# Kernel optimization log

Hardware: AMD Instinct MI355X
Metric: run time of the kernel (lower is better)

Reference implementation:

```python
import jax, jax.numpy as jnp
import numpy as np

HID = 4096
BLOCK = 64


def _masks(n=HID, bs=BLOCK):
    blk = jnp.arange(n) // bs
    mask_diag = (blk[:, None] == blk[None, :]).astype(jnp.float32)  # block-diagonal ones
    triu = (jnp.arange(n)[:, None] <= jnp.arange(n)[None, :]).astype(jnp.float32)
    mask_triu = triu * (1.0 - mask_diag)  # strictly above-block upper triangle
    return mask_diag, mask_triu


def _mc_linear(x, W, b, mask_diag, mask_triu):
    # A uses detached input (stop_gradient); B carries gradient through x.
    A = jax.lax.stop_gradient(x) @ (W * mask_triu)
    B = x @ (W * mask_diag)
    return A + B + b


def setup_inputs() -> dict:
    key = jax.random.key(0)
    ks = jax.random.split(key, 10)
    X = jax.random.normal(ks[0], (8192, 1024), dtype=jnp.float32)
    s_in = 1.0 / np.sqrt(1024)
    s_h = 1.0 / np.sqrt(HID)
    W0 = jax.random.normal(ks[1], (1024, HID), dtype=jnp.float32) * s_in
    b0 = jax.random.normal(ks[2], (HID,), dtype=jnp.float32) * s_in
    W1 = jax.random.normal(ks[3], (HID, HID), dtype=jnp.float32) * s_h
    b1 = jax.random.normal(ks[4], (HID,), dtype=jnp.float32) * s_h
    W2 = jax.random.normal(ks[5], (HID, HID), dtype=jnp.float32) * s_h
    b2 = jax.random.normal(ks[6], (HID,), dtype=jnp.float32) * s_h
    W3 = jax.random.normal(ks[7], (HID, HID), dtype=jnp.float32) * s_h
    b3 = jax.random.normal(ks[8], (HID,), dtype=jnp.float32) * s_h
    return {"X": X, "W0": W0, "b0": b0, "W1": W1, "b1": b1,
            "W2": W2, "b2": b2, "W3": W3, "b3": b3}


def reference(X, W0, b0, W1, b1, W2, b2, W3, b3):
    mask_diag, mask_triu = _masks()
    h = X @ W0 + b0  # [B, HID]
    for W, b in ((W1, b1), (W2, b2), (W3, b3)):
        h = jax.nn.relu(h)  # dropout=0.0 -> identity
        h = _mc_linear(h, W, b, mask_diag, mask_triu)
    y_pred = h[..., BLOCK - 1::BLOCK]  # [B, num_blocks]
    return y_pred[..., -1]  # level = -1 (default LEVEL)
```

## Files before the change

kernel.cpp:

```cpp
#include <hip/hip_runtime.h>

typedef unsigned short u16;
typedef __attribute__((ext_vector_type(8))) short short8;
typedef __attribute__((ext_vector_type(4))) float f32x4;
typedef __attribute__((ext_vector_type(4))) unsigned short us4;

__device__ __forceinline__ u16 f2bf(float f) {
    unsigned u = __float_as_uint(f);
    u += 0x7fffu + ((u >> 16) & 1u);
    return (u16)(u >> 16);
}
__device__ __forceinline__ float bf2f(u16 h) {
    return __uint_as_float(((unsigned)h) << 16);
}

__global__ __launch_bounds__(256) void k_cvt(const float* __restrict__ in,
                                             u16* __restrict__ out, long n) {
    long i = ((long)blockIdx.x * 256 + threadIdx.x) * 4;
    if (i >= n) return;
    float4 v = *(const float4*)(in + i);
    us4 o;
    o.x = f2bf(v.x); o.y = f2bf(v.y); o.z = f2bf(v.z); o.w = f2bf(v.w);
    *(us4*)(out + i) = o;
}

__global__ __launch_bounds__(256) void k_transpose(const float* __restrict__ W,
                                                   u16* __restrict__ Wt,
                                                   int K, int N, int mask) {
    __shared__ float tile[32][33];
    const int n0 = blockIdx.x * 32, k0 = blockIdx.y * 32;
    const int tx = threadIdx.x, ty = threadIdx.y;
    if (mask && ((k0 >> 6) > (n0 >> 6))) {
        if (k0 >= ((n0 >> 8) + 1) * 256) return;
#pragma unroll
        for (int j = 0; j < 32; j += 8)
            Wt[(size_t)(n0 + ty + j) * K + (k0 + tx)] = 0;
        return;
    }
#pragma unroll
    for (int j = 0; j < 32; j += 8)
        tile[ty + j][tx] = W[(size_t)(k0 + ty + j) * N + (n0 + tx)];
    __syncthreads();
#pragma unroll
    for (int j = 0; j < 32; j += 8)
        Wt[(size_t)(n0 + ty + j) * K + (k0 + tx)] = f2bf(tile[tx][ty + j]);
}

__global__ __launch_bounds__(256) void k_extract(const float* __restrict__ W3,
                                                 float* __restrict__ col, int N) {
    int k = blockIdx.x * 256 + threadIdx.x;
    col[k] = W3[(size_t)k * N + (N - 1)];
}

#define BM 256
#define BN 256
#define BK 32
#define BUFE 16384
#define GLDS(src, dst)                                                          \
    __builtin_amdgcn_global_load_lds(                                           \
        (const __attribute__((address_space(1))) void*)(src),                   \
        (__attribute__((address_space(3))) void*)(dst), 16, 0, 0)

__global__ __launch_bounds__(512, 2) void k_gemm(const u16* __restrict__ A,
                                                 const u16* __restrict__ Bt,
                                                 const float* __restrict__ bias,
                                                 u16* __restrict__ C,
                                                 int M, int N, int K, int varK) {
    __shared__ __align__(16) u16 lds[4 * BUFE];

    const int d = blockIdx.y * gridDim.x + blockIdx.x;
    int bx, by;
    if (varK) {
        bx = (int)gridDim.x - 1 - (d / (int)gridDim.y);
        by = d % (int)gridDim.y;
    } else {
        const int nwg = (int)(gridDim.x * gridDim.y);
        const int cpx = nwg >> 3;
        const int swz = (d & 7) * cpx + (d >> 3);
        bx = swz % (int)gridDim.x;
        by = swz / (int)gridDim.x;
    }

    const int tid = (int)threadIdx.x;
    const int lane = tid & 63, wv = tid >> 6;
    const int wm = wv >> 2, wn = wv & 3;
    const int keff = varK ? min(K, (bx + 1) * BN) : K;
    const int nt = keff >> 5;

    const u16* Ab = A + (size_t)by * BM * K;
    const u16* Bb = Bt + (size_t)bx * BN * K;

    const int c0 = tid, c1 = tid + 512;
    const int ar0 = c0 >> 2, as0 = ((c0 & 3) ^ ((c0 >> 3) & 3)) * 8;
    const int ar1 = c1 >> 2, as1 = ((c1 & 3) ^ ((c1 >> 3) & 3)) * 8;
    const u16* pA0 = Ab + (size_t)ar0 * K + as0;
    const u16* pA1 = Ab + (size_t)ar1 * K + as1;
    const u16* pB0 = Bb + (size_t)ar0 * K + as0;
    const u16* pB1 = Bb + (size_t)ar1 * K + as1;
    u16* dA0 = lds + c0 * 8;
    u16* dA1 = lds + c1 * 8;
    u16* dB0 = lds + 8192 + c0 * 8;
    u16* dB1 = lds + 8192 + c1 * 8;

    const int l15 = lane & 15;
    const int sl8 = (((lane >> 4) ^ ((l15 >> 1) & 3))) * 8;
    const int aoff = (wm * 128 + l15) * BK + sl8;
    const int boff = 8192 + (wn * 64 + l15) * BK + sl8;

#define STAGE(t)                                                      \
    {                                                                 \
        const size_t o = (size_t)(t)*BK;                              \
        const int b = ((t)&3) * BUFE;                                 \
        GLDS(pA0 + o, dA0 + b); GLDS(pA1 + o, dA1 + b);               \
        GLDS(pB0 + o, dB0 + b); GLDS(pB1 + o, dB1 + b);               \
    }
#define DSREAD(t, af, bf)                                             \
    {                                                                 \
        const int b = ((t)&3) * BUFE;                                 \
        _Pragma("unroll")                                             \
        for (int mf = 0; mf < 8; ++mf)                                \
            af[mf] = *(const short8*)(lds + b + aoff + mf * 512);     \
        _Pragma("unroll")                                             \
        for (int nf = 0; nf < 4; ++nf)                                \
            bf[nf] = *(const short8*)(lds + b + boff + nf * 512);     \
    }
#define MFMA_SET(af, bf)                                              \
    {                                                                 \
        __builtin_amdgcn_s_setprio(1);                                \
        _Pragma("unroll")                                             \
        for (int mf = 0; mf < 8; ++mf)                                \
            _Pragma("unroll")                                         \
            for (int nf = 0; nf < 4; ++nf)                            \
                acc[mf][nf] = __builtin_amdgcn_mfma_f32_16x16x32_bf16(\
                    af[mf], bf[nf], acc[mf][nf], 0, 0, 0);            \
        __builtin_amdgcn_s_setprio(0);                                \
    }
#define WAITBAR4  asm volatile("s_waitcnt vmcnt(4)\n\ts_barrier" ::: "memory")
#define WAITBAR0  asm volatile("s_waitcnt vmcnt(0)\n\ts_barrier" ::: "memory")

    f32x4 acc[8][4];
#pragma unroll
    for (int i = 0; i < 8; ++i)
#pragma unroll
        for (int j = 0; j < 4; ++j)
            acc[i][j] = (f32x4){0.f, 0.f, 0.f, 0.f};

    short8 afA[8], bfA[4], afB[8], bfB[4];

    STAGE(0); STAGE(1); STAGE(2);
    WAITBAR4;
    DSREAD(0, afA, bfA);

    for (int t = 0; t < nt; t += 2) {
        if (t + 3 < nt) STAGE(t + 3);
        DSREAD(t + 1, afB, bfB);
        MFMA_SET(afA, bfA);
        if (t + 3 < nt) WAITBAR4; else WAITBAR0;
        const int u = t + 1;
        if (u + 3 < nt) STAGE(u + 3);
        if (u + 1 < nt) DSREAD(u + 1, afA, bfA);
        MFMA_SET(afB, bfB);
        if (u + 1 < nt) { if (u + 3 < nt) WAITBAR4; else WAITBAR0; }
    }

    const int rbase = by * BM + wm * 128 + (lane >> 4) * 4;
    const int cbase = bx * BN + wn * 64 + l15;
#pragma unroll
    for (int nf = 0; nf < 4; ++nf) {
        const int gc = cbase + nf * 16;
        const float bv = bias[gc];
#pragma unroll
        for (int mf = 0; mf < 8; ++mf) {
#pragma unroll
            for (int r = 0; r < 4; ++r) {
                int gr = rbase + mf * 16 + r;
                float h = acc[mf][nf][r] + bv;
                h = fmaxf(h, 0.0f);
                C[(size_t)gr * N + gc] = f2bf(h);
            }
        }
    }
#undef STAGE
#undef DSREAD
#undef MFMA_SET
#undef WAITBAR4
#undef WAITBAR0
}

__global__ __launch_bounds__(256) void k_matvec(const u16* __restrict__ act,
                                                const float* __restrict__ col,
                                                const float* __restrict__ b3,
                                                float* __restrict__ out, int K) {
    const int m = blockIdx.x, t = (int)threadIdx.x;
    const u16* row = act + (size_t)m * K;
    float acc = 0.f;
#pragma unroll
    for (int j = 0; j < 2; ++j) {
        int base = t * 16 + j * 8;
        short8 v = *(const short8*)(row + base);
#pragma unroll
        for (int u = 0; u < 8; ++u)
            acc += bf2f((u16)v[u]) * col[base + u];
    }
#pragma unroll
    for (int off = 32; off > 0; off >>= 1)
        acc += __shfl_down(acc, off);
    __shared__ float red[4];
    if ((t & 63) == 0) red[t >> 6] = acc;
    __syncthreads();
    if (t == 0) out[m] = red[0] + red[1] + red[2] + red[3] + b3[K - 1];
}

extern "C" void kernel_launch(void* const* d_in, const int* in_sizes, int n_in,
                              void* d_out, int out_size, void* d_ws, size_t ws_size,
                              hipStream_t stream) {
    const float* X  = (const float*)d_in[0];
    const float* W0 = (const float*)d_in[1];
    const float* b0 = (const float*)d_in[2];
    const float* W1 = (const float*)d_in[3];
    const float* b1 = (const float*)d_in[4];
    const float* W2 = (const float*)d_in[5];
    const float* b2 = (const float*)d_in[6];
    const float* W3 = (const float*)d_in[7];
    const float* b3 = (const float*)d_in[8];
    float* out = (float*)d_out;

    const int M = 8192, K0 = 1024, H = 4096;

    char* ws = (char*)d_ws;
    u16* Wt    = (u16*)(ws);
    u16* actA  = (u16*)(ws + 33554432);
    u16* actB  = (u16*)(ws + 33554432 + 67108864);
    u16* Xb    = actB;
    float* col = (float*)(ws + 33554432 + 2 * 67108864);

    k_cvt<<<dim3((M * K0) / 1024), 256, 0, stream>>>(X, Xb, (long)M * K0);
    k_transpose<<<dim3(H / 32, K0 / 32), dim3(32, 8), 0, stream>>>(W0, Wt, K0, H, 0);
    k_gemm<<<dim3(H / BN, M / BM), 512, 0, stream>>>(Xb, Wt, b0, actA, M, H, K0, 0);
    k_transpose<<<dim3(H / 32, H / 32), dim3(32, 8), 0, stream>>>(W1, Wt, H, H, 1);
    k_gemm<<<dim3(H / BN, M / BM), 512, 0, stream>>>(actA, Wt, b1, actB, M, H, H, 1);
    k_transpose<<<dim3(H / 32, H / 32), dim3(32, 8), 0, stream>>>(W2, Wt, H, H, 1);
    k_gemm<<<dim3(H / BN, M / BM), 512, 0, stream>>>(actB, Wt, b2, actA, M, H, H, 1);
    k_extract<<<dim3(H / 256), 256, 0, stream>>>(W3, col, H);
    k_matvec<<<dim3(M), 256, 0, stream>>>(actA, col, b3, out, H);
}
```

Baseline: 413.0 us.

## Restructure GEMM main loop to BK=64 double buffer with interleaved sub-stage loads

Raises the K-tile from 32 to 64 and replaces the 4-deep BK=32 ring with a 2-buffer BK=64 scheme. Each tile is split into four MFMA quarter-steps, and the global-to-LDS loads for the next tile (A chunks, and B for the tile after) are interleaved between them with finer barriers. It also uses a new 8-way XOR LDS swizzle. The aim is fewer barrier round-trips per K element and better overlap of loads with MFMA. The cost is more barriers per tile and a more fragile scheduling of buffer reuse hazards.

```diff
diff --git a/kernel.cpp b/kernel.cpp
--- a/kernel.cpp
+++ b/kernel.cpp
@@ -54,8 +54,7 @@
 
 #define BM 256
 #define BN 256
-#define BK 32
-#define BUFE 16384
+#define BK 64
 #define GLDS(src, dst)                                                          \
     __builtin_amdgcn_global_load_lds(                                           \
         (const __attribute__((address_space(1))) void*)(src),                   \
@@ -66,7 +65,7 @@
                                                  const float* __restrict__ bias,
                                                  u16* __restrict__ C,
                                                  int M, int N, int K, int varK) {
-    __shared__ __align__(16) u16 lds[4 * BUFE];
+    __shared__ __align__(16) u16 lds[2 * 32768];
 
     const int d = blockIdx.y * gridDim.x + blockIdx.x;
     int bx, by;
@@ -85,58 +84,58 @@
     const int lane = tid & 63, wv = tid >> 6;
     const int wm = wv >> 2, wn = wv & 3;
     const int keff = varK ? min(K, (bx + 1) * BN) : K;
-    const int nt = keff >> 5;
+    const int nt = keff >> 6;
 
     const u16* Ab = A + (size_t)by * BM * K;
     const u16* Bb = Bt + (size_t)bx * BN * K;
 
-    const int c0 = tid, c1 = tid + 512;
-    const int ar0 = c0 >> 2, as0 = ((c0 & 3) ^ ((c0 >> 3) & 3)) * 8;
-    const int ar1 = c1 >> 2, as1 = ((c1 & 3) ^ ((c1 >> 3) & 3)) * 8;
-    const u16* pA0 = Ab + (size_t)ar0 * K + as0;
-    const u16* pA1 = Ab + (size_t)ar1 * K + as1;
-    const u16* pB0 = Bb + (size_t)ar0 * K + as0;
-    const u16* pB1 = Bb + (size_t)ar1 * K + as1;
-    u16* dA0 = lds + c0 * 8;
-    u16* dA1 = lds + c1 * 8;
-    u16* dB0 = lds + 8192 + c0 * 8;
-    u16* dB1 = lds + 8192 + c1 * 8;
+    const int tr = tid >> 3, ts = tid & 7;
+    const int ss = ts ^ (tr & 7);
+    const u16* aSrc = Ab + (size_t)tr * K + ss * 8;
+    const u16* bSrc = Bb + (size_t)tr * K + ss * 8;
+
+#define STA(tt, ci, dbuf) GLDS(aSrc + (size_t)(tt) * BK + (size_t)(ci) * 64 * K, \
+                               lds + (dbuf) + (ci) * 4096 + tid * 8)
+#define STB(tt, ci, dbuf) GLDS(bSrc + (size_t)(tt) * BK + (size_t)(ci) * 64 * K, \
+                               lds + (dbuf) + 16384 + (ci) * 4096 + tid * 8)
 
     const int l15 = lane & 15;
-    const int sl8 = (((lane >> 4) ^ ((l15 >> 1) & 3))) * 8;
-    const int aoff = (wm * 128 + l15) * BK + sl8;
-    const int boff = 8192 + (wn * 64 + l15) * BK + sl8;
-
-#define STAGE(t)                                                      \
-    {                                                                 \
-        const size_t o = (size_t)(t)*BK;                              \
-        const int b = ((t)&3) * BUFE;                                 \
-        GLDS(pA0 + o, dA0 + b); GLDS(pA1 + o, dA1 + b);               \
-        GLDS(pB0 + o, dB0 + b); GLDS(pB1 + o, dB1 + b);               \
-    }
-#define DSREAD(t, af, bf)                                             \
-    {                                                                 \
-        const int b = ((t)&3) * BUFE;                                 \
-        _Pragma("unroll")                                             \
-        for (int mf = 0; mf < 8; ++mf)                                \
-            af[mf] = *(const short8*)(lds + b + aoff + mf * 512);     \
-        _Pragma("unroll")                                             \
-        for (int nf = 0; nf < 4; ++nf)                                \
-            bf[nf] = *(const short8*)(lds + b + boff + nf * 512);     \
-    }
-#define MFMA_SET(af, bf)                                              \
-    {                                                                 \
-        __builtin_amdgcn_s_setprio(1);                                \
-        _Pragma("unroll")                                             \
-        for (int mf = 0; mf < 8; ++mf)                                \
-            _Pragma("unroll")                                         \
-            for (int nf = 0; nf < 4; ++nf)                            \
-                acc[mf][nf] = __builtin_amdgcn_mfma_f32_16x16x32_bf16(\
-                    af[mf], bf[nf], acc[mf][nf], 0, 0, 0);            \
-        __builtin_amdgcn_s_setprio(0);                                \
-    }
-#define WAITBAR4  asm volatile("s_waitcnt vmcnt(4)\n\ts_barrier" ::: "memory")
-#define WAITBAR0  asm volatile("s_waitcnt vmcnt(0)\n\ts_barrier" ::: "memory")
+    const int sw = (lane >> 4) ^ (l15 & 7);
+    const int arow = wm * 128 + l15;
+    const int brow = wn * 64 + l15;
+
+#define RDA(dst, mfh, ks, dbuf)                                                        \
+    {                                                                                  \
+        _Pragma("unroll")                                                              \
+        for (int i = 0; i < 4; ++i)                                                    \
+            dst[i] = *(const short8*)(lds + (dbuf) + (arow + (mfh) * 64 + i * 16) * 64 \
+                                      + ((sw ^ ((ks) << 2))) * 8);                     \
+    }
+#define RDB(dst, ks, dbuf)                                                             \
+    {                                                                                  \
+        _Pragma("unroll")                                                              \
+        for (int nf = 0; nf < 4; ++nf)                                                 \
+            dst[nf] = *(const short8*)(lds + (dbuf) + 16384 + (brow + nf * 16) * 64    \
+                                       + ((sw ^ ((ks) << 2))) * 8);                    \
+    }
+#define MFMA16(afS, bfS, mb)                                                           \
+    {                                                                                  \
+        __builtin_amdgcn_s_setprio(1);                                                 \
+        _Pragma("unroll")                                                              \
+        for (int i = 0; i < 4; ++i)                                                    \
+            _Pragma("unroll")                                                          \
+            for (int nf = 0; nf < 4; ++nf)                                             \
+                acc[(mb) + i][nf] = __builtin_amdgcn_mfma_f32_16x16x32_bf16(           \
+                    afS[i], bfS[nf], acc[(mb) + i][nf], 0, 0, 0);                      \
+        __builtin_amdgcn_s_setprio(0);                                                 \
+    }
+#define MIDSYNC                                                   \
+    __builtin_amdgcn_s_barrier();                                 \
+    asm volatile("s_waitcnt lgkmcnt(0)" ::: "memory");            \
+    __builtin_amdgcn_sched_barrier(0);
+#define ENDSYNC                                                   \
+    asm volatile("s_waitcnt vmcnt(2)" ::: "memory");              \
+    __builtin_amdgcn_s_barrier();
 
     f32x4 acc[8][4];
 #pragma unroll
@@ -145,22 +144,43 @@
         for (int j = 0; j < 4; ++j)
             acc[i][j] = (f32x4){0.f, 0.f, 0.f, 0.f};
 
-    short8 afA[8], bfA[4], afB[8], bfB[4];
-
-    STAGE(0); STAGE(1); STAGE(2);
-    WAITBAR4;
-    DSREAD(0, afA, bfA);
-
-    for (int t = 0; t < nt; t += 2) {
-        if (t + 3 < nt) STAGE(t + 3);
-        DSREAD(t + 1, afB, bfB);
-        MFMA_SET(afA, bfA);
-        if (t + 3 < nt) WAITBAR4; else WAITBAR0;
-        const int u = t + 1;
-        if (u + 3 < nt) STAGE(u + 3);
-        if (u + 1 < nt) DSREAD(u + 1, afA, bfA);
-        MFMA_SET(afB, bfB);
-        if (u + 1 < nt) { if (u + 3 < nt) WAITBAR4; else WAITBAR0; }
+    short8 afX[4], afY[4], bfA[4], bfB[4];
+
+    STA(0, 0, 0); STA(0, 2, 0); STA(0, 1, 0); STA(0, 3, 0);
+    STB(0, 0, 0); STB(0, 1, 0); STB(0, 2, 0); STB(0, 3, 0);
+    STB(1, 0, 32768); STB(1, 1, 32768); STB(1, 2, 32768); STB(1, 3, 32768);
+    asm volatile("s_waitcnt vmcnt(4)" ::: "memory");
+    __builtin_amdgcn_s_barrier();
+    RDA(afX, 0, 0, 0);
+    RDB(bfA, 0, 0);
+
+    for (int T = 0; T < nt; ++T) {
+        const int bT = (T & 1) << 15;
+        const int bNx = bT ^ 32768;
+        RDA(afY, 1, 0, bT);
+        if (T + 1 < nt) { STA(T + 1, 0, bNx); STA(T + 1, 2, bNx); }
+        MIDSYNC;
+        MFMA16(afX, bfA, 0);
+        ENDSYNC;
+        RDA(afX, 0, 1, bT);
+        RDB(bfB, 1, bT);
+        if (T + 1 < nt) { STA(T + 1, 1, bNx); STA(T + 1, 3, bNx); }
+        MIDSYNC;
+        MFMA16(afY, bfA, 4);
+        ENDSYNC;
+        RDA(afY, 1, 1, bT);
+        if (T + 2 < nt) { STB(T + 2, 0, bT); STB(T + 2, 1, bT); }
+        MIDSYNC;
+        MFMA16(afX, bfB, 0);
+        ENDSYNC;
+        if (T + 1 < nt) {
+            RDA(afX, 0, 0, bNx);
+            RDB(bfA, 0, bNx);
+        }
+        if (T + 2 < nt) { STB(T + 2, 2, bT); STB(T + 2, 3, bT); }
+        MIDSYNC;
+        MFMA16(afY, bfB, 4);
+        ENDSYNC;
     }
 
     const int rbase = by * BM + wm * 128 + (lane >> 4) * 4;
@@ -180,11 +200,13 @@
             }
         }
     }
-#undef STAGE
-#undef DSREAD
-#undef MFMA_SET
-#undef WAITBAR4
-#undef WAITBAR0
+#undef STA
+#undef STB
+#undef RDA
+#undef RDB
+#undef MFMA16
+#undef MIDSYNC
+#undef ENDSYNC
 }
 
 __global__ __launch_bounds__(256) void k_matvec(const u16* __restrict__ act,
```

After: 387.4 us. -6.2%, faster.

## Split GEMM main loop into four half-tile phases with interleaved loads

Applied to the files above, without the earlier changes.

Restructures the bf16 MFMA GEMM main loop so that each K-tile is processed in two half-M phases. Each phase has its own LDS reads, global-to-LDS stages and barriers, so A and B global loads are spread across phases and interleaved with smaller 16-MFMA groups. This keeps fewer fragment registers live (4 A fragments at a time instead of 8) and is meant to improve overlap of memory traffic with compute, at the cost of more barriers per tile. The LDS swizzle and addressing are also recomputed in a different form.

```diff
diff --git a/kernel.cpp b/kernel.cpp
--- a/kernel.cpp
+++ b/kernel.cpp
@@ -90,53 +90,52 @@
     const u16* Ab = A + (size_t)by * BM * K;
     const u16* Bb = Bt + (size_t)bx * BN * K;
 
-    const int c0 = tid, c1 = tid + 512;
-    const int ar0 = c0 >> 2, as0 = ((c0 & 3) ^ ((c0 >> 3) & 3)) * 8;
-    const int ar1 = c1 >> 2, as1 = ((c1 & 3) ^ ((c1 >> 3) & 3)) * 8;
-    const u16* pA0 = Ab + (size_t)ar0 * K + as0;
-    const u16* pA1 = Ab + (size_t)ar1 * K + as1;
-    const u16* pB0 = Bb + (size_t)ar0 * K + as0;
-    const u16* pB1 = Bb + (size_t)ar1 * K + as1;
-    u16* dA0 = lds + c0 * 8;
-    u16* dA1 = lds + c1 * 8;
-    u16* dB0 = lds + 8192 + c0 * 8;
-    u16* dB1 = lds + 8192 + c1 * 8;
+    const int tr = tid >> 2, ts = tid & 3;
+    const int ss = ts ^ ((tr >> 1) & 3);
+    const u16* aSrc = Ab + (size_t)tr * K + ss * 8;
+    const u16* bSrc = Bb + (size_t)tr * K + ss * 8;
+
+#define STA(tt, ci, dbuf) GLDS(aSrc + (size_t)(tt) * BK + (size_t)(ci) * 128 * K, \
+                               lds + (dbuf) + (ci) * 4096 + tid * 8)
+#define STB(tt, ci, dbuf) GLDS(bSrc + (size_t)(tt) * BK + (size_t)(ci) * 128 * K, \
+                               lds + (dbuf) + 8192 + (ci) * 4096 + tid * 8)
 
     const int l15 = lane & 15;
-    const int sl8 = (((lane >> 4) ^ ((l15 >> 1) & 3))) * 8;
-    const int aoff = (wm * 128 + l15) * BK + sl8;
-    const int boff = 8192 + (wn * 64 + l15) * BK + sl8;
-
-#define STAGE(t)                                                      \
-    {                                                                 \
-        const size_t o = (size_t)(t)*BK;                              \
-        const int b = ((t)&3) * BUFE;                                 \
-        GLDS(pA0 + o, dA0 + b); GLDS(pA1 + o, dA1 + b);               \
-        GLDS(pB0 + o, dB0 + b); GLDS(pB1 + o, dB1 + b);               \
-    }
-#define DSREAD(t, af, bf)                                             \
-    {                                                                 \
-        const int b = ((t)&3) * BUFE;                                 \
-        _Pragma("unroll")                                             \
-        for (int mf = 0; mf < 8; ++mf)                                \
-            af[mf] = *(const short8*)(lds + b + aoff + mf * 512);     \
-        _Pragma("unroll")                                             \
-        for (int nf = 0; nf < 4; ++nf)                                \
-            bf[nf] = *(const short8*)(lds + b + boff + nf * 512);     \
-    }
-#define MFMA_SET(af, bf)                                              \
-    {                                                                 \
-        __builtin_amdgcn_s_setprio(1);                                \
-        _Pragma("unroll")                                             \
-        for (int mf = 0; mf < 8; ++mf)                                \
-            _Pragma("unroll")                                         \
-            for (int nf = 0; nf < 4; ++nf)                            \
-                acc[mf][nf] = __builtin_amdgcn_mfma_f32_16x16x32_bf16(\
-                    af[mf], bf[nf], acc[mf][nf], 0, 0, 0);            \
-        __builtin_amdgcn_s_setprio(0);                                \
-    }
-#define WAITBAR4  asm volatile("s_waitcnt vmcnt(4)\n\ts_barrier" ::: "memory")
-#define WAITBAR0  asm volatile("s_waitcnt vmcnt(0)\n\ts_barrier" ::: "memory")
+    const int sw = (lane >> 4) ^ ((l15 >> 1) & 3);
+    const int arow = wm * 128 + l15;
+    const int brow = wn * 64 + l15;
+
+#define RDA(dst, mfh, dbuf)                                                          \
+    {                                                                                \
+        _Pragma("unroll")                                                            \
+        for (int i = 0; i < 4; ++i)                                                  \
+            dst[i] = *(const short8*)(lds + (dbuf) + (arow + (mfh) * 64 + i * 16) * 32 \
+                                      + sw * 8);                                     \
+    }
+#define RDB(dst, dbuf)                                                               \
+    {                                                                                \
+        _Pragma("unroll")                                                            \
+        for (int nf = 0; nf < 4; ++nf)                                               \
+            dst[nf] = *(const short8*)(lds + (dbuf) + 8192 + (brow + nf * 16) * 32   \
+                                       + sw * 8);                                    \
+    }
+#define MFMA16(afS, bfS, mb)                                                         \
+    {                                                                                \
+        __builtin_amdgcn_s_setprio(1);                                              \
+        _Pragma("unroll")                                                            \
+        for (int i = 0; i < 4; ++i)                                                  \
+            _Pragma("unroll")                                                        \
+            for (int nf = 0; nf < 4; ++nf)                                           \
+                acc[(mb) + i][nf] = __builtin_amdgcn_mfma_f32_16x16x32_bf16(         \
+                    afS[i], bfS[nf], acc[(mb) + i][nf], 0, 0, 0);                    \
+        __builtin_amdgcn_s_setprio(0);                                              \
+    }
+#define PHASE_END                                                 \
+    __builtin_amdgcn_sched_barrier(0);                            \
+    asm volatile("s_barrier" ::: "memory");
+#define VMW6 asm volatile("s_waitcnt vmcnt(6)" ::: "memory")
+#define VMW4 asm volatile("s_waitcnt vmcnt(4)" ::: "memory")
+#define VMW0 asm volatile("s_waitcnt vmcnt(0)" ::: "memory")
 
     f32x4 acc[8][4];
 #pragma unroll
@@ -145,22 +144,47 @@
         for (int j = 0; j < 4; ++j)
             acc[i][j] = (f32x4){0.f, 0.f, 0.f, 0.f};
 
-    short8 afA[8], bfA[4], afB[8], bfB[4];
-
-    STAGE(0); STAGE(1); STAGE(2);
-    WAITBAR4;
-    DSREAD(0, afA, bfA);
-
-    for (int t = 0; t < nt; t += 2) {
-        if (t + 3 < nt) STAGE(t + 3);
-        DSREAD(t + 1, afB, bfB);
-        MFMA_SET(afA, bfA);
-        if (t + 3 < nt) WAITBAR4; else WAITBAR0;
-        const int u = t + 1;
-        if (u + 3 < nt) STAGE(u + 3);
-        if (u + 1 < nt) DSREAD(u + 1, afA, bfA);
-        MFMA_SET(afB, bfB);
-        if (u + 1 < nt) { if (u + 3 < nt) WAITBAR4; else WAITBAR0; }
+    short8 afX[4], afY[4], bfP[4], bfQ[4];
+
+    STA(0, 0, 0);     STA(0, 1, 0);     STB(0, 0, 0);     STB(0, 1, 0);
+    STA(1, 0, BUFE);  STA(1, 1, BUFE);  STB(1, 0, BUFE);  STB(1, 1, BUFE);
+    STA(2, 0, 2*BUFE);STA(2, 1, 2*BUFE);STB(2, 0, 2*BUFE);STB(2, 1, 2*BUFE);
+    asm volatile("s_waitcnt vmcnt(8)" ::: "memory");
+    asm volatile("s_barrier" ::: "memory");
+    RDA(afX, 0, 0);
+    RDB(bfP, 0);
+
+    for (int T = 0; T < nt; T += 2) {
+        const int U = T + 1;
+        const int bT = (T & 3) * BUFE;
+        const int bU = ((T + 1) & 3) * BUFE;
+        const int bV = ((T + 2) & 3) * BUFE;
+        const int bZ1 = ((T + 3) & 3) * BUFE;
+        const int bZ2 = ((T + 4) & 3) * BUFE;
+        RDA(afY, 1, bT);
+        if (T + 3 < nt) { STA(T + 3, 0, bZ1); STA(T + 3, 1, bZ1); }
+        MFMA16(afX, bfP, 0);
+        if (T + 3 < nt) { VMW6; } else { VMW0; }
+        PHASE_END;
+        RDA(afX, 0, bU);
+        RDB(bfQ, bU);
+        if (T + 3 < nt) { STB(T + 3, 0, bZ1); STB(T + 3, 1, bZ1); }
+        MFMA16(afY, bfP, 4);
+        PHASE_END;
+        RDA(afY, 1, bU);
+        if (U + 3 < nt) { STA(U + 3, 0, bZ2); STA(U + 3, 1, bZ2); }
+        MFMA16(afX, bfQ, 0);
+        if (U + 1 < nt) {
+            if (U + 3 < nt) { VMW6; } else if (U + 2 < nt) { VMW4; } else { VMW0; }
+        }
+        PHASE_END;
+        if (U + 1 < nt) {
+            RDA(afX, 0, bV);
+            RDB(bfP, bV);
+        }
+        if (U + 3 < nt) { STB(U + 3, 0, bZ2); STB(U + 3, 1, bZ2); }
+        MFMA16(afY, bfQ, 4);
+        PHASE_END;
     }
 
     const int rbase = by * BM + wm * 128 + (lane >> 4) * 4;
@@ -180,11 +204,15 @@
             }
         }
     }
-#undef STAGE
-#undef DSREAD
-#undef MFMA_SET
-#undef WAITBAR4
-#undef WAITBAR0
+#undef STA
+#undef STB
+#undef RDA
+#undef RDB
+#undef MFMA16
+#undef PHASE_END
+#undef VMW6
+#undef VMW4
+#undef VMW0
 }
 
 __global__ __launch_bounds__(256) void k_matvec(const u16* __restrict__ act,
```

Result: faster. 393.2 us (-4.8%).

## Restructure GEMM main loop into BK=64 double buffer with quarter-phase interleaving

Applied to the files above, without the earlier changes.

Replaces the 4-stage BK=32 LDS ring with a 2-buffer BK=64 layout split into half-K slabs. Each K tile runs as four phases that interleave LDS reads, async global-to-LDS stages and quarter-tile MFMA blocks, separated by explicit barriers and sched_barriers. It keeps a smaller fragment register set live (4 A fragments instead of 16). The aim is finer overlap of loads with compute and lower register pressure, at the cost of many more workgroup barriers per iteration and tighter prefetch timing.

```diff
diff --git a/kernel.cpp b/kernel.cpp
--- a/kernel.cpp
+++ b/kernel.cpp
@@ -54,8 +54,8 @@
 
 #define BM 256
 #define BN 256
-#define BK 32
-#define BUFE 16384
+#define BK 64
+#define BUFE 32768
 #define GLDS(src, dst)                                                          \
     __builtin_amdgcn_global_load_lds(                                           \
         (const __attribute__((address_space(1))) void*)(src),                   \
@@ -66,7 +66,7 @@
                                                  const float* __restrict__ bias,
                                                  u16* __restrict__ C,
                                                  int M, int N, int K, int varK) {
-    __shared__ __align__(16) u16 lds[4 * BUFE];
+    __shared__ __align__(16) u16 lds[2 * BUFE];
 
     const int d = blockIdx.y * gridDim.x + blockIdx.x;
     int bx, by;
@@ -85,58 +85,66 @@
     const int lane = tid & 63, wv = tid >> 6;
     const int wm = wv >> 2, wn = wv & 3;
     const int keff = varK ? min(K, (bx + 1) * BN) : K;
-    const int nt = keff >> 5;
+    const int nt = keff >> 6;
 
     const u16* Ab = A + (size_t)by * BM * K;
     const u16* Bb = Bt + (size_t)bx * BN * K;
 
-    const int c0 = tid, c1 = tid + 512;
-    const int ar0 = c0 >> 2, as0 = ((c0 & 3) ^ ((c0 >> 3) & 3)) * 8;
-    const int ar1 = c1 >> 2, as1 = ((c1 & 3) ^ ((c1 >> 3) & 3)) * 8;
-    const u16* pA0 = Ab + (size_t)ar0 * K + as0;
-    const u16* pA1 = Ab + (size_t)ar1 * K + as1;
-    const u16* pB0 = Bb + (size_t)ar0 * K + as0;
-    const u16* pB1 = Bb + (size_t)ar1 * K + as1;
-    u16* dA0 = lds + c0 * 8;
-    u16* dA1 = lds + c1 * 8;
-    u16* dB0 = lds + 8192 + c0 * 8;
-    u16* dB1 = lds + 8192 + c1 * 8;
+    const int srow = tid >> 2, sslot = tid & 3;
+    const int ss = sslot ^ ((srow >> 1) & 3);
+    const u16* aSrc0 = Ab + (size_t)srow * K + ss * 8;
+    const u16* aSrc1 = Ab + (size_t)(srow + 128) * K + ss * 8;
+    const u16* bSrc0 = Bb + (size_t)srow * K + ss * 8;
+    const u16* bSrc1 = Bb + (size_t)(srow + 128) * K + ss * 8;
+
+#define STGA(tt, kh)                                                            \
+    {                                                                           \
+        const int db = (((tt) & 1) * BUFE) + (kh) * 8192;                       \
+        const size_t so = (size_t)(tt) * 64 + (kh) * 32;                        \
+        GLDS(aSrc0 + so, lds + db + tid * 8);                                   \
+        GLDS(aSrc1 + so, lds + db + 4096 + tid * 8);                            \
+    }
+#define STGB(tt, kh)                                                            \
+    {                                                                           \
+        const int db = (((tt) & 1) * BUFE) + 16384 + (kh) * 8192;               \
+        const size_t so = (size_t)(tt) * 64 + (kh) * 32;                        \
+        GLDS(bSrc0 + so, lds + db + tid * 8);                                   \
+        GLDS(bSrc1 + so, lds + db + 4096 + tid * 8);                            \
+    }
 
     const int l15 = lane & 15;
-    const int sl8 = (((lane >> 4) ^ ((l15 >> 1) & 3))) * 8;
-    const int aoff = (wm * 128 + l15) * BK + sl8;
-    const int boff = 8192 + (wn * 64 + l15) * BK + sl8;
-
-#define STAGE(t)                                                      \
-    {                                                                 \
-        const size_t o = (size_t)(t)*BK;                              \
-        const int b = ((t)&3) * BUFE;                                 \
-        GLDS(pA0 + o, dA0 + b); GLDS(pA1 + o, dA1 + b);               \
-        GLDS(pB0 + o, dB0 + b); GLDS(pB1 + o, dB1 + b);               \
-    }
-#define DSREAD(t, af, bf)                                             \
-    {                                                                 \
-        const int b = ((t)&3) * BUFE;                                 \
-        _Pragma("unroll")                                             \
-        for (int mf = 0; mf < 8; ++mf)                                \
-            af[mf] = *(const short8*)(lds + b + aoff + mf * 512);     \
-        _Pragma("unroll")                                             \
-        for (int nf = 0; nf < 4; ++nf)                                \
-            bf[nf] = *(const short8*)(lds + b + boff + nf * 512);     \
-    }
-#define MFMA_SET(af, bf)                                              \
-    {                                                                 \
-        __builtin_amdgcn_s_setprio(1);                                \
-        _Pragma("unroll")                                             \
-        for (int mf = 0; mf < 8; ++mf)                                \
-            _Pragma("unroll")                                         \
-            for (int nf = 0; nf < 4; ++nf)                            \
-                acc[mf][nf] = __builtin_amdgcn_mfma_f32_16x16x32_bf16(\
-                    af[mf], bf[nf], acc[mf][nf], 0, 0, 0);            \
-        __builtin_amdgcn_s_setprio(0);                                \
-    }
-#define WAITBAR4  asm volatile("s_waitcnt vmcnt(4)\n\ts_barrier" ::: "memory")
-#define WAITBAR0  asm volatile("s_waitcnt vmcnt(0)\n\ts_barrier" ::: "memory")
+    const int sw = (lane >> 4) ^ ((l15 >> 1) & 3);
+    const int arow = wm * 128 + l15;
+    const int brow = wn * 64 + l15;
+
+#define RDA(mh, ks, bT)                                                         \
+    {                                                                           \
+        _Pragma("unroll")                                                       \
+        for (int i = 0; i < 4; ++i)                                             \
+            af[i] = *(const short8*)(lds + (bT) + (ks) * 8192 +                  \
+                                     (arow + (mh) * 64 + i * 16) * 32 + sw * 8);\
+    }
+#define RDB(ks, bT)                                                             \
+    {                                                                           \
+        _Pragma("unroll")                                                       \
+        for (int nf = 0; nf < 4; ++nf)                                          \
+            bf[nf] = *(const short8*)(lds + (bT) + 16384 + (ks) * 8192 +        \
+                                      (brow + nf * 16) * 32 + sw * 8);          \
+    }
+#define MFMAQ(mh)                                                               \
+    {                                                                           \
+        __builtin_amdgcn_s_setprio(1);                                          \
+        _Pragma("unroll")                                                       \
+        for (int i = 0; i < 4; ++i)                                             \
+            _Pragma("unroll")                                                   \
+            for (int nf = 0; nf < 4; ++nf)                                      \
+                acc[(mh) * 4 + i][nf] = __builtin_amdgcn_mfma_f32_16x16x32_bf16(\
+                    af[i], bf[nf], acc[(mh) * 4 + i][nf], 0, 0, 0);             \
+        __builtin_amdgcn_s_setprio(0);                                          \
+    }
+#define SB __builtin_amdgcn_sched_barrier(0)
+#define BAR __builtin_amdgcn_s_barrier()
+#define LGKM0 { SB; asm volatile("s_waitcnt lgkmcnt(0)"); SB; }
 
     f32x4 acc[8][4];
 #pragma unroll
@@ -145,22 +153,45 @@
         for (int j = 0; j < 4; ++j)
             acc[i][j] = (f32x4){0.f, 0.f, 0.f, 0.f};
 
-    short8 afA[8], bfA[4], afB[8], bfB[4];
-
-    STAGE(0); STAGE(1); STAGE(2);
-    WAITBAR4;
-    DSREAD(0, afA, bfA);
-
-    for (int t = 0; t < nt; t += 2) {
-        if (t + 3 < nt) STAGE(t + 3);
-        DSREAD(t + 1, afB, bfB);
-        MFMA_SET(afA, bfA);
-        if (t + 3 < nt) WAITBAR4; else WAITBAR0;
-        const int u = t + 1;
-        if (u + 3 < nt) STAGE(u + 3);
-        if (u + 1 < nt) DSREAD(u + 1, afA, bfA);
-        MFMA_SET(afB, bfB);
-        if (u + 1 < nt) { if (u + 3 < nt) WAITBAR4; else WAITBAR0; }
+    short8 af[4], bf[4];
+
+    STGA(0, 0); STGA(0, 1); STGB(0, 0); STGB(0, 1);
+    STGA(1, 0); STGB(1, 0); STGB(1, 1);
+    SB; asm volatile("s_waitcnt vmcnt(6)"); SB;
+    BAR; SB;
+
+    for (int T = 0; T < nt; ++T) {
+        const int bT = (T & 1) * BUFE;
+        RDA(0, 0, bT);
+        RDB(0, bT);
+        if (T + 1 < nt) STGA(T + 1, 1);
+        SB; BAR;
+        LGKM0;
+        MFMAQ(0);
+        SB; BAR;
+        RDA(1, 0, bT);
+        if (T + 2 < nt) STGB(T + 2, 0);
+        SB; BAR;
+        LGKM0;
+        MFMAQ(1);
+        SB; BAR;
+        RDA(0, 1, bT);
+        RDB(1, bT);
+        if (T + 2 < nt) STGA(T + 2, 0);
+        SB; BAR;
+        LGKM0;
+        MFMAQ(0);
+        SB; BAR;
+        RDA(1, 1, bT);
+        if (T + 2 < nt) STGB(T + 2, 1);
+        if (T + 1 < nt) {
+            if (T + 2 < nt) { SB; asm volatile("s_waitcnt vmcnt(6)"); SB; }
+            else            { SB; asm volatile("s_waitcnt vmcnt(0)"); SB; }
+        }
+        SB; BAR;
+        LGKM0;
+        MFMAQ(1);
+        SB; BAR;
     }
 
     const int rbase = by * BM + wm * 128 + (lane >> 4) * 4;
@@ -180,11 +211,14 @@
             }
         }
     }
-#undef STAGE
-#undef DSREAD
-#undef MFMA_SET
-#undef WAITBAR4
-#undef WAITBAR0
+#undef STGA
+#undef STGB
+#undef RDA
+#undef RDB
+#undef MFMAQ
+#undef SB
+#undef BAR
+#undef LGKM0
 }
 
 __global__ __launch_bounds__(256) void k_matvec(const u16* __restrict__ act,
```

After: 404.9 us. Within noise of the previous version (-2.0%).
